# Performance work log

Measured on AMD Instinct MI355X. Metric: run time of the kernel, lower is better.

## Reference

```python
import jax, jax.numpy as jnp
import numpy as np


def setup_inputs() -> dict:
    key = jax.random.key(0)
    k1, k2 = jax.random.split(key)
    B, D1, D2 = 32768, 1024, 4096
    g1 = jax.random.normal(k1, (B, D1), dtype=jnp.float32)
    # Learned parameter, initialized as in the module: N(0,1)*0.02 + 0.2
    W = jax.random.normal(k2, (D1, D2), dtype=jnp.float32) * 0.02 + 0.2
    return {"g1": g1, "W": W}


def reference(g1, W):
    beta = 10.0
    # Column-normalize W: each column divided by its L2 norm. [d1, d2]
    nc = jnp.sqrt(jnp.sum(W ** 2, axis=0, keepdims=True))
    nW = W / nc
    # Similarity scores. [B, d2]
    x2 = g1 @ nW
    # Scaled logsumexp energy. [B]
    return -1.0 / beta * jax.nn.logsumexp(beta * x2, axis=-1)
```

## Files before the change

### kernel.cpp

```cpp
#include <hip/hip_runtime.h>
#include <hip/hip_bf16.h>
#include <hip/hip_fp8.h>

typedef int i32x8 __attribute__((ext_vector_type(8)));
typedef int i32x4 __attribute__((ext_vector_type(4)));
typedef float f32x4 __attribute__((ext_vector_type(4)));
typedef unsigned char uchar_t;

constexpr int NB = 32768;
constexpr int D1 = 1024;
constexpr int D2 = 4096;
constexpr float BETA_LOG2E = 14.4269504088896340736f;
constexpr float SCALE_A = 16.0f;
constexpr float SCALE_B = 8192.0f;
constexpr float INV_SCALE = 1.0f / (16.0f * 8192.0f);

__device__ __forceinline__ uchar_t f32_to_fp8(float f) {
  __hip_fp8_e4m3 q(f);
  return (uchar_t)q.__x;
}

__device__ __forceinline__ void async_copy16(const void* g, void* l) {
  __builtin_amdgcn_global_load_lds(
      (const __attribute__((address_space(1))) void*)g,
      (__attribute__((address_space(3))) void*)l, 16, 0, 0);
}

__global__ void colstats(const float* __restrict__ W, float* __restrict__ sq,
                         float* __restrict__ colsum) {
  int j = blockIdx.x * 256 + threadIdx.x;
  int k0 = blockIdx.y * 64;
  float a = 0.f, b = 0.f;
#pragma unroll 8
  for (int k = 0; k < 64; ++k) {
    float w = W[(size_t)(k0 + k) * D2 + j];
    a += w * w; b += w;
  }
  atomicAdd(&sq[j], a);
  atomicAdd(&colsum[j], b);
}

__global__ void convert_a(const float* __restrict__ g1, uchar_t* __restrict__ A8,
                          float* __restrict__ S) {
  int row = blockIdx.x;
  int t = threadIdx.x;
  const float* src = g1 + (size_t)row * D1 + t * 8;
  float v[8];
  *(float4*)(v)     = *(const float4*)(src);
  *(float4*)(v + 4) = *(const float4*)(src + 4);
  float sum = 0.f;
  union { uchar_t b[8]; uint2 u; } o;
#pragma unroll
  for (int j = 0; j < 8; ++j) { sum += v[j]; o.b[j] = f32_to_fp8(v[j] * SCALE_A); }
  *(uint2*)(A8 + (size_t)row * D1 + t * 8) = o.u;
#pragma unroll
  for (int m = 1; m < 64; m <<= 1) sum += __shfl_xor(sum, m, 64);
  __shared__ float part[2];
  if ((t & 63) == 0) part[t >> 6] = sum;
  __syncthreads();
  if (t == 0) S[row] = part[0] + part[1];
}

__global__ void convert_b(const float* __restrict__ W, const float* __restrict__ sq,
                          const float* __restrict__ colsum,
                          uchar_t* __restrict__ B8t, float* __restrict__ mu) {
  __shared__ float tile[64][65];
  int t = threadIdx.x;
  int j0 = blockIdx.x * 64;
  int k0 = blockIdx.y * 64;
  int c = t & 63, r4 = t >> 6;
#pragma unroll
  for (int s = 0; s < 16; ++s) {
    int k = s * 4 + r4;
    tile[k][c] = W[(size_t)(k0 + k) * D2 + j0 + c];
  }
  __syncthreads();
#pragma unroll
  for (int s = 0; s < 16; ++s) {
    int jj = s * 4 + r4;
    float inv = 1.0f / sqrtf(sq[j0 + jj]);
    float muj = colsum[j0 + jj] * inv * (1.0f / 1024.0f);
    if (k0 == 0 && c == 0) mu[j0 + jj] = muj;
    float dw = tile[c][jj] * inv - muj;
    B8t[(size_t)(j0 + jj) * D1 + k0 + c] = f32_to_fp8(dw * SCALE_B);
  }
}

__global__ __launch_bounds__(256, 2)
void gemm_expsum(const uchar_t* __restrict__ A8, const uchar_t* __restrict__ B8t,
                 const float* __restrict__ S, const float* __restrict__ mu,
                 float* __restrict__ s) {
  __shared__ __align__(16) uchar_t As[2 * 128 * 128];
  __shared__ __align__(16) uchar_t Bs[2 * 128 * 128];

  const int t = threadIdx.x;
  const int row0 = blockIdx.y * 128;
  const int col0 = blockIdx.x * 128;
  const int lane = t & 63;
  const int wave = t >> 6;
  const int wm = (wave >> 1) * 64;
  const int wn = (wave & 1) * 64;
  const int llo = lane & 15, lhi = lane >> 4;

  f32x4 acc[4][4] = {};

  const int srow = t >> 3;
  const int sseg = (t & 7) ^ (srow & 7);
  const uchar_t* gA = A8  + (size_t)(row0 + srow) * D1 + sseg * 16;
  const uchar_t* gB = B8t + (size_t)(col0 + srow) * D1 + sseg * 16;

  const int sw0 = ((lhi * 2 + 0) ^ (llo & 7)) * 16;
  const int sw1 = ((lhi * 2 + 1) ^ (llo & 7)) * 16;

#pragma unroll
  for (int i = 0; i < 4; ++i) {
    async_copy16(gA + (size_t)i * 32 * D1, As + t * 16 + i * 4096);
    async_copy16(gB + (size_t)i * 32 * D1, Bs + t * 16 + i * 4096);
  }

  int p = 0;
  for (int kt = 0; kt < D1; kt += 128, p ^= 1) {
    __syncthreads();
    if (kt + 128 < D1) {
#pragma unroll
      for (int i = 0; i < 4; ++i) {
        async_copy16(gA + (size_t)i * 32 * D1 + kt + 128,
                     As + (p ^ 1) * 16384 + t * 16 + i * 4096);
        async_copy16(gB + (size_t)i * 32 * D1 + kt + 128,
                     Bs + (p ^ 1) * 16384 + t * 16 + i * 4096);
      }
    }
    const uchar_t* baseA = As + p * 16384;
    const uchar_t* baseB = Bs + p * 16384;
    i32x8 af[4], bq[4];
#pragma unroll
    for (int mi = 0; mi < 4; ++mi) {
      const uchar_t* q = baseA + (wm + mi * 16 + llo) * 128;
      i32x4 h0 = *(const i32x4*)(q + sw0);
      i32x4 h1 = *(const i32x4*)(q + sw1);
      af[mi] = __builtin_shufflevector(h0, h1, 0, 1, 2, 3, 4, 5, 6, 7);
    }
#pragma unroll
    for (int ni = 0; ni < 4; ++ni) {
      const uchar_t* q = baseB + (wn + ni * 16 + llo) * 128;
      i32x4 h0 = *(const i32x4*)(q + sw0);
      i32x4 h1 = *(const i32x4*)(q + sw1);
      bq[ni] = __builtin_shufflevector(h0, h1, 0, 1, 2, 3, 4, 5, 6, 7);
    }
#pragma unroll
    for (int mi = 0; mi < 4; ++mi)
#pragma unroll
      for (int ni = 0; ni < 4; ++ni)
        acc[mi][ni] = __builtin_amdgcn_mfma_scale_f32_16x16x128_f8f6f4(
            af[mi], bq[ni], acc[mi][ni],
            0, 0,
            0, 127,
            0, 127);
  }

  float muv[4];
#pragma unroll
  for (int ni = 0; ni < 4; ++ni) muv[ni] = mu[col0 + wn + ni * 16 + llo];

#pragma unroll
  for (int mi = 0; mi < 4; ++mi) {
    const int row = row0 + wm + mi * 16 + lhi * 4;
    float4 sv = *(const float4*)(S + row);
    float sarr[4] = {sv.x, sv.y, sv.z, sv.w};
    float rs[4];
#pragma unroll
    for (int r = 0; r < 4; ++r) {
      float v = 0.f;
#pragma unroll
      for (int ni = 0; ni < 4; ++ni) {
        float x2 = fmaf(acc[mi][ni][r], INV_SCALE, muv[ni] * sarr[r]);
        v += exp2f(x2 * BETA_LOG2E);
      }
      rs[r] = v;
    }
#pragma unroll
    for (int m = 1; m < 16; m <<= 1) {
#pragma unroll
      for (int r = 0; r < 4; ++r)
        rs[r] += __shfl_xor(rs[r], m, 64);
    }
    if (llo == 0) {
#pragma unroll
      for (int r = 0; r < 4; ++r)
        atomicAdd(&s[row + r], rs[r]);
    }
  }
}

__global__ void finish_kernel(const float* __restrict__ s, float* __restrict__ out) {
  int b = blockIdx.x * 256 + threadIdx.x;
  out[b] = -0.1f * logf(s[b]);
}

extern "C" void kernel_launch(void* const* d_in, const int* in_sizes, int n_in,
                              void* d_out, int out_size, void* d_ws, size_t ws_size,
                              hipStream_t stream) {
  const float* g1 = (const float*)d_in[0];
  const float* W  = (const float*)d_in[1];
  float* out = (float*)d_out;

  char* ws = (char*)d_ws;
  float* s       = (float*)ws;
  float* sq      = (float*)(ws + 131072);
  float* colsum  = (float*)(ws + 147456);
  float* mu      = (float*)(ws + 163840);
  float* S       = (float*)(ws + 180224);
  uchar_t* A8    = (uchar_t*)(ws + 311296);
  uchar_t* B8t   = (uchar_t*)(ws + 311296 + 33554432);

  hipMemsetAsync(ws, 0, 180224, stream);

  colstats<<<dim3(16, 16), 256, 0, stream>>>(W, sq, colsum);
  convert_b<<<dim3(64, 16), 256, 0, stream>>>(W, sq, colsum, B8t, mu);
  convert_a<<<dim3(32768), 128, 0, stream>>>(g1, A8, S);
  gemm_expsum<<<dim3(32, 256), 256, 0, stream>>>(A8, B8t, S, mu, s);
  finish_kernel<<<dim3(128), 256, 0, stream>>>(s, out);
}
```

Baseline: 421.0 us.

## Merge A and B conversion kernels and use packed hardware FP8 conversion

Fuses the g1 and W quantization kernels into one launch, with blocks split by index between the two jobs. The A conversion becomes a grid-stride, one-wave-per-row loop with coalesced float4 loads, and each row's sum is reduced by wave shuffles instead of shared memory. FP8 conversion now uses the packed cvt_pk_fp8_f32 builtin instead of the software constructor. This cuts a kernel launch and conversion instruction cost, at some risk of different rounding or saturation from the hardware conversion.

```diff
diff --git a/kernel.cpp b/kernel.cpp
--- a/kernel.cpp
+++ b/kernel.cpp
@@ -16,8 +16,7 @@
 constexpr float INV_SCALE = 1.0f / (16.0f * 8192.0f);
 
 __device__ __forceinline__ uchar_t f32_to_fp8(float f) {
-  __hip_fp8_e4m3 q(f);
-  return (uchar_t)q.__x;
+  return (uchar_t)(__builtin_amdgcn_cvt_pk_fp8_f32(f, f, 0, false) & 0xff);
 }
 
 __device__ __forceinline__ void async_copy16(const void* g, void* l) {
@@ -40,49 +39,59 @@
   atomicAdd(&colsum[j], b);
 }
 
-__global__ void convert_a(const float* __restrict__ g1, uchar_t* __restrict__ A8,
-                          float* __restrict__ S) {
-  int row = blockIdx.x;
-  int t = threadIdx.x;
-  const float* src = g1 + (size_t)row * D1 + t * 8;
-  float v[8];
-  *(float4*)(v)     = *(const float4*)(src);
-  *(float4*)(v + 4) = *(const float4*)(src + 4);
-  float sum = 0.f;
-  union { uchar_t b[8]; uint2 u; } o;
-#pragma unroll
-  for (int j = 0; j < 8; ++j) { sum += v[j]; o.b[j] = f32_to_fp8(v[j] * SCALE_A); }
-  *(uint2*)(A8 + (size_t)row * D1 + t * 8) = o.u;
-#pragma unroll
-  for (int m = 1; m < 64; m <<= 1) sum += __shfl_xor(sum, m, 64);
-  __shared__ float part[2];
-  if ((t & 63) == 0) part[t >> 6] = sum;
-  __syncthreads();
-  if (t == 0) S[row] = part[0] + part[1];
-}
-
-__global__ void convert_b(const float* __restrict__ W, const float* __restrict__ sq,
-                          const float* __restrict__ colsum,
-                          uchar_t* __restrict__ B8t, float* __restrict__ mu) {
+__global__ __launch_bounds__(256)
+void merged_convert(const float* __restrict__ g1, uchar_t* __restrict__ A8,
+                    float* __restrict__ S, const float* __restrict__ W,
+                    const float* __restrict__ sq, const float* __restrict__ colsum,
+                    uchar_t* __restrict__ B8t, float* __restrict__ mu) {
   __shared__ float tile[64][65];
-  int t = threadIdx.x;
-  int j0 = blockIdx.x * 64;
-  int k0 = blockIdx.y * 64;
-  int c = t & 63, r4 = t >> 6;
-#pragma unroll
-  for (int s = 0; s < 16; ++s) {
-    int k = s * 4 + r4;
-    tile[k][c] = W[(size_t)(k0 + k) * D2 + j0 + c];
-  }
-  __syncthreads();
-#pragma unroll
-  for (int s = 0; s < 16; ++s) {
-    int jj = s * 4 + r4;
-    float inv = 1.0f / sqrtf(sq[j0 + jj]);
-    float muj = colsum[j0 + jj] * inv * (1.0f / 1024.0f);
-    if (k0 == 0 && c == 0) mu[j0 + jj] = muj;
-    float dw = tile[c][jj] * inv - muj;
-    B8t[(size_t)(j0 + jj) * D1 + k0 + c] = f32_to_fp8(dw * SCALE_B);
+  if (blockIdx.x < 2048) {
+    const int lane = threadIdx.x & 63;
+    const int gw = (blockIdx.x * 256 + threadIdx.x) >> 6;
+    for (int row = gw; row < NB; row += 8192) {
+      const float4* src = (const float4*)(g1 + (size_t)row * D1);
+      float4 f[4];
+#pragma unroll
+      for (int c = 0; c < 4; ++c) f[c] = src[c * 64 + lane];
+      float sum = 0.f;
+#pragma unroll
+      for (int c = 0; c < 4; ++c) sum += f[c].x + f[c].y + f[c].z + f[c].w;
+      unsigned ob[4];
+#pragma unroll
+      for (int c = 0; c < 4; ++c) {
+        unsigned w = __builtin_amdgcn_cvt_pk_fp8_f32(f[c].x * SCALE_A,
+                                                     f[c].y * SCALE_A, 0, false);
+        ob[c] = __builtin_amdgcn_cvt_pk_fp8_f32(f[c].z * SCALE_A,
+                                                f[c].w * SCALE_A, w, true);
+      }
+      unsigned* dst = (unsigned*)(A8 + (size_t)row * D1);
+#pragma unroll
+      for (int c = 0; c < 4; ++c) dst[c * 64 + lane] = ob[c];
+#pragma unroll
+      for (int m = 1; m < 64; m <<= 1) sum += __shfl_xor(sum, m, 64);
+      if (lane == 0) S[row] = sum;
+    }
+  } else {
+    const int b = blockIdx.x - 2048;
+    const int t = threadIdx.x;
+    const int j0 = (b & 63) * 64;
+    const int k0 = (b >> 6) * 64;
+    const int c = t & 63, r4 = t >> 6;
+#pragma unroll
+    for (int s = 0; s < 16; ++s) {
+      int k = s * 4 + r4;
+      tile[k][c] = W[(size_t)(k0 + k) * D2 + j0 + c];
+    }
+    __syncthreads();
+#pragma unroll
+    for (int s = 0; s < 16; ++s) {
+      int jj = s * 4 + r4;
+      float inv = 1.0f / sqrtf(sq[j0 + jj]);
+      float muj = colsum[j0 + jj] * inv * (1.0f / 1024.0f);
+      if (k0 == 0 && c == 0) mu[j0 + jj] = muj;
+      float dw = tile[c][jj] * inv - muj;
+      B8t[(size_t)(j0 + jj) * D1 + k0 + c] = f32_to_fp8(dw * SCALE_B);
+    }
   }
 }
 
@@ -153,9 +162,7 @@
       for (int ni = 0; ni < 4; ++ni)
         acc[mi][ni] = __builtin_amdgcn_mfma_scale_f32_16x16x128_f8f6f4(
             af[mi], bq[ni], acc[mi][ni],
-            0, 0,
-            0, 127,
-            0, 127);
+            0, 0, 0, 127, 0, 127);
   }
 
   float muv[4];
@@ -216,8 +223,7 @@
   hipMemsetAsync(ws, 0, 180224, stream);
 
   colstats<<<dim3(16, 16), 256, 0, stream>>>(W, sq, colsum);
-  convert_b<<<dim3(64, 16), 256, 0, stream>>>(W, sq, colsum, B8t, mu);
-  convert_a<<<dim3(32768), 128, 0, stream>>>(g1, A8, S);
+  merged_convert<<<dim3(3072), 256, 0, stream>>>(g1, A8, S, W, sq, colsum, B8t, mu);
   gemm_expsum<<<dim3(32, 256), 256, 0, stream>>>(A8, B8t, S, mu, s);
   finish_kernel<<<dim3(128), 256, 0, stream>>>(s, out);
 }
```

Result: no change. 420.5 us (-0.1%).
